# Kernel tuning notes

Hardware: AMD Instinct MI355X
Metric: run time of the kernel (lower is better)

## Reference

```python
import jax, jax.numpy as jnp
import numpy as np

N, ID, OD, M, S, L = 65536, 16, 8, 1024, 8, 64


def setup_inputs() -> dict:
    key = jax.random.key(0)
    k1, k2, k3, k4, k5, k6 = jax.random.split(key, 6)
    return {
        "x": jax.random.normal(k1, (N, ID), dtype=jnp.float32),
        "inducing_locations": jax.random.uniform(k2, (M, ID), dtype=jnp.float32),
        "inducing_weights": jax.random.normal(k3, (S, OD, M), dtype=jnp.float32),
        "prior_frequency": jax.random.normal(k4, (OD, ID, L), dtype=jnp.float32),
        "prior_phase": jax.random.uniform(k5, (OD, L), dtype=jnp.float32, maxval=2 * np.pi),
        "prior_weights": jax.random.normal(k6, (S, OD, L), dtype=jnp.float32),
    }


def _rbf_matrix(x, z):
    # ExponentiatedQuadratic with amplitude=1, length_scale=1:
    # k(x,z) = exp(-0.5 * ||x - z||^2)
    x2 = jnp.sum(x * x, axis=-1)[:, None]          # [N,1]
    z2 = jnp.sum(z * z, axis=-1)[None, :]          # [1,M]
    sq = jnp.maximum(x2 + z2 - 2.0 * (x @ z.T), 0.0)
    return jnp.exp(-0.5 * sq)                      # [N,M]


def reference(x, inducing_locations, inducing_weights, prior_frequency, prior_phase, prior_weights):
    # ---- prior (random Fourier features) ----
    # spectral_weights for unit RBF: outer_weights = ones((OD,L)), inner_weights = ones((ID,))
    # rescaled_x = x / 1 = x
    # basis_fn_inner_prod: [OD, N, L]
    inner = jnp.einsum('ni,oil->onl', x, prior_frequency)
    basis_fn = jnp.cos(inner + prior_phase[:, None, :])              # [OD,N,L]
    basis_weight = jnp.sqrt(2.0 / prior_frequency.shape[-1]) * prior_weights  # [S,OD,L]
    f_prior = jnp.einsum('onl,sol->son', basis_fn, basis_weight)     # [S,OD,N]

    # ---- data term (kernel matrix + matvec) ----
    K = _rbf_matrix(x, inducing_locations)                           # [N,M]
    f_data = jnp.einsum('nm,som->son', K, inducing_weights)          # [S,OD,N]

    return f_prior + f_data
```

## Files before the change

kernel.cpp:

```cpp
#include <hip/hip_runtime.h>
#include <hip/hip_bf16.h>

#define N_PTS 65536
#define LOG2E 1.4426950408889634f

typedef __attribute__((ext_vector_type(8))) short short8;
typedef __attribute__((ext_vector_type(4))) float float4v;

#if __has_builtin(__builtin_amdgcn_exp2f)
#define EXP2F(x) __builtin_amdgcn_exp2f(x)
#else
#define EXP2F(x) exp2f(x)
#endif

__device__ __forceinline__ short f2b(float f) {
    __hip_bfloat16 h = __float2bfloat16(f);
    return *(short*)&h;
}
__device__ __forceinline__ float b2f(short s) {
    __hip_bfloat16 h = *(__hip_bfloat16*)&s;
    return __bfloat162float(h);
}

__device__ __forceinline__ int permrow(int p) {
    return ((p & 12) << 1) + (p & 3) + ((p >> 4) << 2);
}

__global__ __launch_bounds__(256) void prep_kernel(
    const float* __restrict__ z, const float* __restrict__ W,
    const float* __restrict__ F, const float* __restrict__ pw,
    const float* __restrict__ ph,
    short* __restrict__ zb, short* __restrict__ FbB,
    short* __restrict__ BWd, short* __restrict__ Wtb,
    float* __restrict__ nz2P, float* __restrict__ phP)
{
    int t = blockIdx.x * 256 + threadIdx.x;
    if (t < 16384) {
        int row = t >> 4, i = t & 15;
        int src = (row & ~31) + permrow(row & 31);
        zb[t] = f2b(LOG2E * z[src * 16 + i]);
    } else if (t < 17408) {
        int m = t - 16384;
        int src = (m & ~31) + permrow(m & 31);
        const float4v* zp = (const float4v*)(z + (size_t)src * 16);
        float s = 0.f;
        #pragma unroll
        for (int k = 0; k < 4; k++) {
            float4v v = zp[k];
            float a0 = b2f(f2b(v.x)), a1 = b2f(f2b(v.y));
            float a2 = b2f(f2b(v.z)), a3 = b2f(f2b(v.w));
            s += a0 * a0 + a1 * a1 + a2 * a2 + a3 * a3;
        }
        nz2P[m] = -(0.5f * LOG2E * s);
    } else if (t < 25600) {
        int p = t - 17408;
        int row = p >> 4, i = p & 15;
        int srow = (row & ~31) + permrow(row & 31);
        int o = srow >> 6, l = srow & 63;
        FbB[p] = f2b(F[o * 1024 + i * 64 + l]);
    } else if (t < 58368) {
        int p = t - 25600;
        int so = p >> 9, ol = p & 511, o = ol >> 6;
        float v = ((so & 7) == o) ? 0.17677669529663687f * pw[so * 64 + (ol & 63)] : 0.f;
        BWd[p] = f2b(v);
    } else if (t < 123904) {
        int p = t - 58368;
        Wtb[p] = f2b(W[p]);
    } else {
        int j = t - 123904;
        int sj = (j & ~31) + permrow(j & 31);
        phP[j] = ph[sj];
    }
}

__global__ __launch_bounds__(256, 4) void fused_kernel(
    const float* __restrict__ x,
    const short* __restrict__ zb, const short* __restrict__ FbB,
    const short* __restrict__ BWd, const short* __restrict__ Wtb,
    const float* __restrict__ nz2P, const float* __restrict__ phP,
    float* __restrict__ out)
{
    __shared__ float x2c[64];
    __shared__ __align__(16) float rbufA[64 * 68];
    __shared__ __align__(16) float rbufB[64 * 68];

    const int tid = threadIdx.x;
    const int lane = tid & 63, w = tid >> 6;
    const int q = lane >> 4, c = lane & 15;
    const int n0 = blockIdx.x * 64;

    if (tid < 64) {
        float s = 0.f;
        const float4v* xr = (const float4v*)(x + (size_t)(n0 + tid) * 16);
        #pragma unroll
        for (int k = 0; k < 4; k++) {
            float4v v = xr[k];
            float a0 = b2f(f2b(v.x)), a1 = b2f(f2b(v.y));
            float a2 = b2f(f2b(v.z)), a3 = b2f(f2b(v.w));
            s += a0 * a0 + a1 * a1 + a2 * a2 + a3 * a3;
        }
        x2c[tid] = 0.5f * LOG2E * s;
    }

    short8 ax[4];
    #pragma unroll
    for (int nt = 0; nt < 4; nt++) {
        ax[nt] = (short8)0;
        if (q < 2) {
            const float4v* xp = (const float4v*)(x + (size_t)(n0 + nt * 16 + c) * 16 + q * 8);
            float4v v0 = xp[0], v1 = xp[1];
            ax[nt][0] = f2b(v0.x); ax[nt][1] = f2b(v0.y);
            ax[nt][2] = f2b(v0.z); ax[nt][3] = f2b(v0.w);
            ax[nt][4] = f2b(v1.x); ax[nt][5] = f2b(v1.y);
            ax[nt][6] = f2b(v1.z); ax[nt][7] = f2b(v1.w);
        }
    }

    float4v acc[4][4];
    #pragma unroll
    for (int a = 0; a < 4; a++)
        #pragma unroll
        for (int nt = 0; nt < 4; nt++) acc[a][nt] = (float4v)(0.f);

    __syncthreads();

    const int mbase = w * 256;
    #pragma unroll 2
    for (int mb = 0; mb < 8; mb++) {
        const int m0 = mbase + mb * 32;
        short8 bzA = (short8)0, bzB = (short8)0;
        if (q < 2) {
            bzA = *(const short8*)(zb + (size_t)(m0 + c) * 16 + q * 8);
            bzB = *(const short8*)(zb + (size_t)(m0 + 16 + c) * 16 + q * 8);
        }
        float4v c0A = *(const float4v*)(nz2P + m0 + 4 * q);
        float4v c0B = *(const float4v*)(nz2P + m0 + 16 + 4 * q);
        short8 pb[4];
        #pragma unroll
        for (int nt = 0; nt < 4; nt++) {
            float4v dA = __builtin_amdgcn_mfma_f32_16x16x32_bf16(bzA, ax[nt], c0A, 0, 0, 0);
            float4v dB = __builtin_amdgcn_mfma_f32_16x16x32_bf16(bzB, ax[nt], c0B, 0, 0, 0);
            short8 t;
            t[0] = f2b(EXP2F(dA[0])); t[1] = f2b(EXP2F(dA[1]));
            t[2] = f2b(EXP2F(dA[2])); t[3] = f2b(EXP2F(dA[3]));
            t[4] = f2b(EXP2F(dB[0])); t[5] = f2b(EXP2F(dB[1]));
            t[6] = f2b(EXP2F(dB[2])); t[7] = f2b(EXP2F(dB[3]));
            pb[nt] = t;
        }
        #pragma unroll
        for (int a = 0; a < 4; a++) {
            short8 aw = *(const short8*)(Wtb + (size_t)(a * 16 + c) * 1024 + m0 + q * 8);
            #pragma unroll
            for (int nt = 0; nt < 4; nt++)
                acc[a][nt] = __builtin_amdgcn_mfma_f32_16x16x32_bf16(aw, pb[nt], acc[a][nt], 0, 0, 0);
        }
    }

    #pragma unroll
    for (int nt = 0; nt < 4; nt++) {
        float sxv = EXP2F(-x2c[nt * 16 + c]);
        #pragma unroll
        for (int a = 0; a < 4; a++) acc[a][nt] *= sxv;
    }

    const int lbase = w * 128;
    #pragma unroll 2
    for (int lb = 0; lb < 4; lb++) {
        const int l0 = lbase + lb * 32;
        short8 bfA = (short8)0, bfB = (short8)0;
        if (q < 2) {
            bfA = *(const short8*)(FbB + (size_t)(l0 + c) * 16 + q * 8);
            bfB = *(const short8*)(FbB + (size_t)(l0 + 16 + c) * 16 + q * 8);
        }
        float4v c0A = *(const float4v*)(phP + l0 + 4 * q);
        float4v c0B = *(const float4v*)(phP + l0 + 16 + 4 * q);
        short8 pb[4];
        #pragma unroll
        for (int nt = 0; nt < 4; nt++) {
            float4v dA = __builtin_amdgcn_mfma_f32_16x16x32_bf16(bfA, ax[nt], c0A, 0, 0, 0);
            float4v dB = __builtin_amdgcn_mfma_f32_16x16x32_bf16(bfB, ax[nt], c0B, 0, 0, 0);
            short8 t;
            t[0] = f2b(__cosf(dA[0])); t[1] = f2b(__cosf(dA[1]));
            t[2] = f2b(__cosf(dA[2])); t[3] = f2b(__cosf(dA[3]));
            t[4] = f2b(__cosf(dB[0])); t[5] = f2b(__cosf(dB[1]));
            t[6] = f2b(__cosf(dB[2])); t[7] = f2b(__cosf(dB[3]));
            pb[nt] = t;
        }
        #pragma unroll
        for (int a = 0; a < 4; a++) {
            short8 aw = *(const short8*)(BWd + (size_t)(a * 16 + c) * 512 + l0 + q * 8);
            #pragma unroll
            for (int nt = 0; nt < 4; nt++)
                acc[a][nt] = __builtin_amdgcn_mfma_f32_16x16x32_bf16(aw, pb[nt], acc[a][nt], 0, 0, 0);
        }
    }

    __syncthreads();
    if (w & 1) {
        float* rb = (w == 1) ? rbufA : rbufB;
        #pragma unroll
        for (int a = 0; a < 4; a++)
            #pragma unroll
            for (int nt = 0; nt < 4; nt++)
                #pragma unroll
                for (int r = 0; r < 4; r++)
                    rb[(a * 16 + 4 * q + r) * 68 + nt * 16 + c] = acc[a][nt][r];
    }
    __syncthreads();
    if (!(w & 1)) {
        float* rb = (w == 0) ? rbufA : rbufB;
        #pragma unroll
        for (int a = 0; a < 4; a++)
            #pragma unroll
            for (int nt = 0; nt < 4; nt++)
                #pragma unroll
                for (int r = 0; r < 4; r++) {
                    int idx = (a * 16 + 4 * q + r) * 68 + nt * 16 + c;
                    rb[idx] += acc[a][nt][r];
                }
    }
    __syncthreads();
    #pragma unroll
    for (int k = 0; k < 16; k++) {
        int idx = k * 256 + tid;
        int row = idx >> 6, nn = idx & 63;
        out[(size_t)row * N_PTS + n0 + nn] = rbufA[row * 68 + nn] + rbufB[row * 68 + nn];
    }
}

extern "C" void kernel_launch(void* const* d_in, const int* in_sizes, int n_in,
                              void* d_out, int out_size, void* d_ws, size_t ws_size,
                              hipStream_t stream) {
    const float* x  = (const float*)d_in[0];
    const float* z  = (const float*)d_in[1];
    const float* W  = (const float*)d_in[2];
    const float* F  = (const float*)d_in[3];
    const float* ph = (const float*)d_in[4];
    const float* pw = (const float*)d_in[5];
    float* out = (float*)d_out;

    char* ws = (char*)d_ws;
    short* zb   = (short*)(ws);
    short* FbB  = (short*)(ws + 32768);
    short* BWd  = (short*)(ws + 49152);
    short* Wtb  = (short*)(ws + 114688);
    float* nz2P = (float*)(ws + 245760);
    float* phP  = (float*)(ws + 249856);

    prep_kernel<<<486, 256, 0, stream>>>(z, W, F, pw, ph, zb, FbB, BWd, Wtb, nz2P, phP);
    fused_kernel<<<1024, 256, 0, stream>>>(x, zb, FbB, BWd, Wtb, nz2P, phP, out);
}
```

Before: 110.9 us.

## Halve points per block and software-prefetch next tile operands in both loops

Each block now handles 32 points instead of 64, doubling the grid to 2048 blocks and halving accumulator registers. Both the kernel-matrix loop and the Fourier-feature loop are fully unrolled, and each iteration loads the next tile's z, bias and weight operands while computing the current one. The aim is to hide global-load latency and raise occupancy and wave count. In exchange, the weight tiles (Wtb, BWd) are re-read per block twice as often, and the extra prefetch registers may offset part of the register saving.

```diff
diff --git a/kernel.cpp b/kernel.cpp
--- a/kernel.cpp
+++ b/kernel.cpp
@@ -80,16 +80,16 @@
     const float* __restrict__ nz2P, const float* __restrict__ phP,
     float* __restrict__ out)
 {
-    __shared__ float x2c[64];
-    __shared__ __align__(16) float rbufA[64 * 68];
-    __shared__ __align__(16) float rbufB[64 * 68];
+    __shared__ float x2c[32];
+    __shared__ __align__(16) float rbufA[64 * 34];
+    __shared__ __align__(16) float rbufB[64 * 34];
 
     const int tid = threadIdx.x;
     const int lane = tid & 63, w = tid >> 6;
     const int q = lane >> 4, c = lane & 15;
-    const int n0 = blockIdx.x * 64;
-
-    if (tid < 64) {
+    const int n0 = blockIdx.x * 32;
+
+    if (tid < 32) {
         float s = 0.f;
         const float4v* xr = (const float4v*)(x + (size_t)(n0 + tid) * 16);
         #pragma unroll
@@ -102,9 +102,9 @@
         x2c[tid] = 0.5f * LOG2E * s;
     }
 
-    short8 ax[4];
-    #pragma unroll
-    for (int nt = 0; nt < 4; nt++) {
+    short8 ax[2];
+    #pragma unroll
+    for (int nt = 0; nt < 2; nt++) {
         ax[nt] = (short8)0;
         if (q < 2) {
             const float4v* xp = (const float4v*)(x + (size_t)(n0 + nt * 16 + c) * 16 + q * 8);
@@ -116,30 +116,57 @@
         }
     }
 
-    float4v acc[4][4];
+    float4v acc[4][2];
     #pragma unroll
     for (int a = 0; a < 4; a++)
         #pragma unroll
-        for (int nt = 0; nt < 4; nt++) acc[a][nt] = (float4v)(0.f);
-
-    __syncthreads();
+        for (int nt = 0; nt < 2; nt++) acc[a][nt] = (float4v)(0.f);
 
     const int mbase = w * 256;
-    #pragma unroll 2
-    for (int mb = 0; mb < 8; mb++) {
-        const int m0 = mbase + mb * 32;
-        short8 bzA = (short8)0, bzB = (short8)0;
+    const int lbase = w * 128;
+
+    short8 bzA = (short8)0, bzB = (short8)0;
+    float4v c0A, c0B;
+    short8 aw0, aw1, aw2, aw3;
+    {
+        const int m0 = mbase;
         if (q < 2) {
             bzA = *(const short8*)(zb + (size_t)(m0 + c) * 16 + q * 8);
             bzB = *(const short8*)(zb + (size_t)(m0 + 16 + c) * 16 + q * 8);
         }
-        float4v c0A = *(const float4v*)(nz2P + m0 + 4 * q);
-        float4v c0B = *(const float4v*)(nz2P + m0 + 16 + 4 * q);
-        short8 pb[4];
-        #pragma unroll
-        for (int nt = 0; nt < 4; nt++) {
-            float4v dA = __builtin_amdgcn_mfma_f32_16x16x32_bf16(bzA, ax[nt], c0A, 0, 0, 0);
-            float4v dB = __builtin_amdgcn_mfma_f32_16x16x32_bf16(bzB, ax[nt], c0B, 0, 0, 0);
+        c0A = *(const float4v*)(nz2P + m0 + 4 * q);
+        c0B = *(const float4v*)(nz2P + m0 + 16 + 4 * q);
+        aw0 = *(const short8*)(Wtb + (size_t)(0 * 16 + c) * 1024 + m0 + q * 8);
+        aw1 = *(const short8*)(Wtb + (size_t)(1 * 16 + c) * 1024 + m0 + q * 8);
+        aw2 = *(const short8*)(Wtb + (size_t)(2 * 16 + c) * 1024 + m0 + q * 8);
+        aw3 = *(const short8*)(Wtb + (size_t)(3 * 16 + c) * 1024 + m0 + q * 8);
+    }
+
+    __syncthreads();
+
+    #pragma unroll
+    for (int mb = 0; mb < 8; mb++) {
+        short8 cbzA = bzA, cbzB = bzB;
+        float4v cc0A = c0A, cc0B = c0B;
+        short8 ca0 = aw0, ca1 = aw1, ca2 = aw2, ca3 = aw3;
+        if (mb < 7) {
+            const int m1 = mbase + (mb + 1) * 32;
+            if (q < 2) {
+                bzA = *(const short8*)(zb + (size_t)(m1 + c) * 16 + q * 8);
+                bzB = *(const short8*)(zb + (size_t)(m1 + 16 + c) * 16 + q * 8);
+            }
+            c0A = *(const float4v*)(nz2P + m1 + 4 * q);
+            c0B = *(const float4v*)(nz2P + m1 + 16 + 4 * q);
+            aw0 = *(const short8*)(Wtb + (size_t)(0 * 16 + c) * 1024 + m1 + q * 8);
+            aw1 = *(const short8*)(Wtb + (size_t)(1 * 16 + c) * 1024 + m1 + q * 8);
+            aw2 = *(const short8*)(Wtb + (size_t)(2 * 16 + c) * 1024 + m1 + q * 8);
+            aw3 = *(const short8*)(Wtb + (size_t)(3 * 16 + c) * 1024 + m1 + q * 8);
+        }
+        short8 pb[2];
+        #pragma unroll
+        for (int nt = 0; nt < 2; nt++) {
+            float4v dA = __builtin_amdgcn_mfma_f32_16x16x32_bf16(cbzA, ax[nt], cc0A, 0, 0, 0);
+            float4v dB = __builtin_amdgcn_mfma_f32_16x16x32_bf16(cbzB, ax[nt], cc0B, 0, 0, 0);
             short8 t;
             t[0] = f2b(EXP2F(dA[0])); t[1] = f2b(EXP2F(dA[1]));
             t[2] = f2b(EXP2F(dA[2])); t[3] = f2b(EXP2F(dA[3]));
@@ -148,37 +175,58 @@
             pb[nt] = t;
         }
         #pragma unroll
-        for (int a = 0; a < 4; a++) {
-            short8 aw = *(const short8*)(Wtb + (size_t)(a * 16 + c) * 1024 + m0 + q * 8);
-            #pragma unroll
-            for (int nt = 0; nt < 4; nt++)
-                acc[a][nt] = __builtin_amdgcn_mfma_f32_16x16x32_bf16(aw, pb[nt], acc[a][nt], 0, 0, 0);
-        }
-    }
-
-    #pragma unroll
-    for (int nt = 0; nt < 4; nt++) {
+        for (int nt = 0; nt < 2; nt++) {
+            acc[0][nt] = __builtin_amdgcn_mfma_f32_16x16x32_bf16(ca0, pb[nt], acc[0][nt], 0, 0, 0);
+            acc[1][nt] = __builtin_amdgcn_mfma_f32_16x16x32_bf16(ca1, pb[nt], acc[1][nt], 0, 0, 0);
+            acc[2][nt] = __builtin_amdgcn_mfma_f32_16x16x32_bf16(ca2, pb[nt], acc[2][nt], 0, 0, 0);
+            acc[3][nt] = __builtin_amdgcn_mfma_f32_16x16x32_bf16(ca3, pb[nt], acc[3][nt], 0, 0, 0);
+        }
+    }
+
+    {
+        const int l0 = lbase;
+        if (q < 2) {
+            bzA = *(const short8*)(FbB + (size_t)(l0 + c) * 16 + q * 8);
+            bzB = *(const short8*)(FbB + (size_t)(l0 + 16 + c) * 16 + q * 8);
+        }
+        c0A = *(const float4v*)(phP + l0 + 4 * q);
+        c0B = *(const float4v*)(phP + l0 + 16 + 4 * q);
+        aw0 = *(const short8*)(BWd + (size_t)(0 * 16 + c) * 512 + l0 + q * 8);
+        aw1 = *(const short8*)(BWd + (size_t)(1 * 16 + c) * 512 + l0 + q * 8);
+        aw2 = *(const short8*)(BWd + (size_t)(2 * 16 + c) * 512 + l0 + q * 8);
+        aw3 = *(const short8*)(BWd + (size_t)(3 * 16 + c) * 512 + l0 + q * 8);
+    }
+
+    #pragma unroll
+    for (int nt = 0; nt < 2; nt++) {
         float sxv = EXP2F(-x2c[nt * 16 + c]);
         #pragma unroll
         for (int a = 0; a < 4; a++) acc[a][nt] *= sxv;
     }
 
-    const int lbase = w * 128;
-    #pragma unroll 2
+    #pragma unroll
     for (int lb = 0; lb < 4; lb++) {
-        const int l0 = lbase + lb * 32;
-        short8 bfA = (short8)0, bfB = (short8)0;
-        if (q < 2) {
-            bfA = *(const short8*)(FbB + (size_t)(l0 + c) * 16 + q * 8);
-            bfB = *(const short8*)(FbB + (size_t)(l0 + 16 + c) * 16 + q * 8);
-        }
-        float4v c0A = *(const float4v*)(phP + l0 + 4 * q);
-        float4v c0B = *(const float4v*)(phP + l0 + 16 + 4 * q);
-        short8 pb[4];
-        #pragma unroll
-        for (int nt = 0; nt < 4; nt++) {
-            float4v dA = __builtin_amdgcn_mfma_f32_16x16x32_bf16(bfA, ax[nt], c0A, 0, 0, 0);
-            float4v dB = __builtin_amdgcn_mfma_f32_16x16x32_bf16(bfB, ax[nt], c0B, 0, 0, 0);
+        short8 cbzA = bzA, cbzB = bzB;
+        float4v cc0A = c0A, cc0B = c0B;
+        short8 ca0 = aw0, ca1 = aw1, ca2 = aw2, ca3 = aw3;
+        if (lb < 3) {
+            const int l1 = lbase + (lb + 1) * 32;
+            if (q < 2) {
+                bzA = *(const short8*)(FbB + (size_t)(l1 + c) * 16 + q * 8);
+                bzB = *(const short8*)(FbB + (size_t)(l1 + 16 + c) * 16 + q * 8);
+            }
+            c0A = *(const float4v*)(phP + l1 + 4 * q);
+            c0B = *(const float4v*)(phP + l1 + 16 + 4 * q);
+            aw0 = *(const short8*)(BWd + (size_t)(0 * 16 + c) * 512 + l1 + q * 8);
+            aw1 = *(const short8*)(BWd + (size_t)(1 * 16 + c) * 512 + l1 + q * 8);
+            aw2 = *(const short8*)(BWd + (size_t)(2 * 16 + c) * 512 + l1 + q * 8);
+            aw3 = *(const short8*)(BWd + (size_t)(3 * 16 + c) * 512 + l1 + q * 8);
+        }
+        short8 pb[2];
+        #pragma unroll
+        for (int nt = 0; nt < 2; nt++) {
+            float4v dA = __builtin_amdgcn_mfma_f32_16x16x32_bf16(cbzA, ax[nt], cc0A, 0, 0, 0);
+            float4v dB = __builtin_amdgcn_mfma_f32_16x16x32_bf16(cbzB, ax[nt], cc0B, 0, 0, 0);
             short8 t;
             t[0] = f2b(__cosf(dA[0])); t[1] = f2b(__cosf(dA[1]));
             t[2] = f2b(__cosf(dA[2])); t[3] = f2b(__cosf(dA[3]));
@@ -187,11 +235,11 @@
             pb[nt] = t;
         }
         #pragma unroll
-        for (int a = 0; a < 4; a++) {
-            short8 aw = *(const short8*)(BWd + (size_t)(a * 16 + c) * 512 + l0 + q * 8);
-            #pragma unroll
-            for (int nt = 0; nt < 4; nt++)
-                acc[a][nt] = __builtin_amdgcn_mfma_f32_16x16x32_bf16(aw, pb[nt], acc[a][nt], 0, 0, 0);
+        for (int nt = 0; nt < 2; nt++) {
+            acc[0][nt] = __builtin_amdgcn_mfma_f32_16x16x32_bf16(ca0, pb[nt], acc[0][nt], 0, 0, 0);
+            acc[1][nt] = __builtin_amdgcn_mfma_f32_16x16x32_bf16(ca1, pb[nt], acc[1][nt], 0, 0, 0);
+            acc[2][nt] = __builtin_amdgcn_mfma_f32_16x16x32_bf16(ca2, pb[nt], acc[2][nt], 0, 0, 0);
+            acc[3][nt] = __builtin_amdgcn_mfma_f32_16x16x32_bf16(ca3, pb[nt], acc[3][nt], 0, 0, 0);
         }
     }
 
@@ -201,10 +249,10 @@
         #pragma unroll
         for (int a = 0; a < 4; a++)
             #pragma unroll
-            for (int nt = 0; nt < 4; nt++)
+            for (int nt = 0; nt < 2; nt++)
                 #pragma unroll
                 for (int r = 0; r < 4; r++)
-                    rb[(a * 16 + 4 * q + r) * 68 + nt * 16 + c] = acc[a][nt][r];
+                    rb[(a * 16 + 4 * q + r) * 34 + nt * 16 + c] = acc[a][nt][r];
     }
     __syncthreads();
     if (!(w & 1)) {
@@ -212,19 +260,19 @@
         #pragma unroll
         for (int a = 0; a < 4; a++)
             #pragma unroll
-            for (int nt = 0; nt < 4; nt++)
+            for (int nt = 0; nt < 2; nt++)
                 #pragma unroll
                 for (int r = 0; r < 4; r++) {
-                    int idx = (a * 16 + 4 * q + r) * 68 + nt * 16 + c;
+                    int idx = (a * 16 + 4 * q + r) * 34 + nt * 16 + c;
                     rb[idx] += acc[a][nt][r];
                 }
     }
     __syncthreads();
     #pragma unroll
-    for (int k = 0; k < 16; k++) {
+    for (int k = 0; k < 8; k++) {
         int idx = k * 256 + tid;
-        int row = idx >> 6, nn = idx & 63;
-        out[(size_t)row * N_PTS + n0 + nn] = rbufA[row * 68 + nn] + rbufB[row * 68 + nn];
+        int row = idx >> 5, nn = idx & 31;
+        out[(size_t)row * N_PTS + n0 + nn] = rbufA[row * 34 + nn] + rbufB[row * 34 + nn];
     }
 }
 
@@ -248,5 +296,5 @@
     float* phP  = (float*)(ws + 249856);
 
     prep_kernel<<<486, 256, 0, stream>>>(z, W, F, pw, ph, zb, FbB, BWd, Wtb, nz2P, phP);
-    fused_kernel<<<1024, 256, 0, stream>>>(x, zb, FbB, BWd, Wtb, nz2P, phP, out);
-}
+    fused_kernel<<<2048, 256, 0, stream>>>(x, zb, FbB, BWd, Wtb, nz2P, phP, out);
+}
```

Result: slower. 126.8 us (+14.3%).
